# Performance work log

Measured on AMD Instinct MI355X. Metric: run time of the kernel, lower is better.

Reference implementation:

```python
import jax, jax.numpy as jnp
import numpy as np

EMBED_DIM = 1024
NUM_HEADS = 16
HEAD_DIM = EMBED_DIM // NUM_HEADS


def setup_inputs() -> dict:
    key = jax.random.key(0)
    ks = jax.random.split(key, 9)
    B, S, E, Hd = 1, 4096, EMBED_DIM, HEAD_DIM
    s = 0.02
    return {
        "x": jax.random.normal(ks[0], (B, S, E), jnp.float32),
        "mask": jnp.ones((B, S, S), jnp.int32),
        "Wq": jax.random.normal(ks[1], (E, E), jnp.float32) * s,
        "bq": jnp.zeros((E,), jnp.float32),
        "Wk": jax.random.normal(ks[2], (E, Hd), jnp.float32) * s,
        "bk": jnp.zeros((Hd,), jnp.float32),
        "Wv": jax.random.normal(ks[3], (E, Hd), jnp.float32) * s,
        "bv": jnp.zeros((Hd,), jnp.float32),
        "Wo": jax.random.normal(ks[4], (E, E), jnp.float32) * s,
        "bo": jnp.zeros((E,), jnp.float32),
    }


def reference(x, mask, Wq, bq, Wk, bk, Wv, bv, Wo, bo):
    B, S, E = x.shape
    H, Hd = NUM_HEADS, HEAD_DIM
    q = (x @ Wq + bq).reshape(B, S, H, Hd).transpose(0, 2, 1, 3)  # [B,H,S,Hd]
    k = x @ Wk + bk  # [B,S,Hd] single KV head (MQA)
    v = x @ Wv + bv  # [B,S,Hd]
    scale = 1.0 / np.sqrt(Hd).astype(np.float32)
    # broadcast single-head K across all query heads
    qk = jnp.einsum('bhqd,bkd->bhqk', q, k) * scale  # [B,H,S,S]
    qk = jnp.where(mask[:, None, :, :] == 0, jnp.float32(-10000.0), qk)
    attn = jax.nn.softmax(qk, axis=-1)
    out = jnp.einsum('bhqk,bkd->bhqd', attn, v)  # [B,H,S,Hd]
    out = out.transpose(0, 2, 1, 3).reshape(B, S, E)
    return out @ Wo + bo
```

## Files before the change

### kernel.cpp

```cpp
#include <hip/hip_runtime.h>
#include <hip/hip_bf16.h>
#include <stdint.h>

typedef __bf16 bf16x8 __attribute__((ext_vector_type(8)));
typedef float f32x4 __attribute__((ext_vector_type(4)));
typedef float f32x16 __attribute__((ext_vector_type(16)));
typedef unsigned int uint2v __attribute__((ext_vector_type(2)));

#define E_DIM 1024
#define HD 64
#define NH 16
#define QKV_LD 1152
#define LOG2E 1.44269504088896f

__device__ __forceinline__ float toF(float x) { return x; }
__device__ __forceinline__ float toF(__hip_bfloat16 x) { return __bfloat162float(x); }
__device__ __forceinline__ void storeOut(float* p, float v) { *p = v; }
__device__ __forceinline__ void storeOut(__hip_bfloat16* p, float v) { *p = __float2bfloat16(v); }

__device__ __forceinline__ unsigned cvtpk_bf16(float lo, float hi_) {
    unsigned r;
    asm("v_cvt_pk_bf16_f32 %0, %1, %2" : "=v"(r) : "v"(lo), "v"(hi_));
    return r;
}
__device__ __forceinline__ void perm32swap(unsigned& a, unsigned& b) {
    uint2v r = __builtin_amdgcn_permlane32_swap(a, b, false, false);
    a = r.x; b = r.y;
}
__device__ __forceinline__ float fexp2(float x) {
    float r;
    asm("v_exp_f32 %0, %1" : "=v"(r) : "v"(x));
    return r;
}

typedef __attribute__((address_space(1))) void gvoid;
typedef __attribute__((address_space(3))) void lvoid;
__device__ __forceinline__ void gload_lds16(const void* g, void* l) {
    __builtin_amdgcn_global_load_lds((gvoid*)g, (lvoid*)l, 16, 0, 0);
}

__global__ void cast_f32_bf16_kernel(const float* __restrict__ in, __hip_bfloat16* __restrict__ o, int n) {
    int i = (blockIdx.x * blockDim.x + threadIdx.x) * 4;
    if (i + 3 < n) {
        float4 v = *reinterpret_cast<const float4*>(in + i);
        __hip_bfloat16 t[4] = {__float2bfloat16(v.x), __float2bfloat16(v.y),
                               __float2bfloat16(v.z), __float2bfloat16(v.w)};
        *reinterpret_cast<uint2*>(o + i) = *reinterpret_cast<uint2*>(t);
    }
}

template<typename InT>
__global__ void transpose_cast_kernel(const InT* __restrict__ in, int ldi,
                                      __hip_bfloat16* __restrict__ out, int ldo,
                                      int R, int C) {
    __shared__ float tile[32][33];
    const int bx = blockIdx.x * 32;
    const int by = blockIdx.y * 32;
    const int tx = threadIdx.x & 31, ty = threadIdx.x >> 5;
#pragma unroll
    for (int j = 0; j < 4; ++j) {
        int r = bx + ty + j * 8, c = by + tx;
        tile[ty + j * 8][tx] = toF(in[(size_t)r * ldi + c]);
    }
    __syncthreads();
#pragma unroll
    for (int j = 0; j < 4; ++j) {
        int c = by + ty + j * 8, r = bx + tx;
        out[(size_t)c * ldo + r] = __float2bfloat16(tile[tx][ty + j * 8]);
    }
}

__global__ __launch_bounds__(256)
void transpose4_kernel(const float* __restrict__ Wq, const float* __restrict__ Wk,
                       const float* __restrict__ Wv, const float* __restrict__ Wo,
                       __hip_bfloat16* __restrict__ wqkvT, __hip_bfloat16* __restrict__ woT) {
    const int z = blockIdx.z;
    const float* in; __hip_bfloat16* out; int ldi;
    if (z == 0)      { in = Wq; out = wqkvT;                                ldi = E_DIM; }
    else if (z == 1) { if (blockIdx.y >= HD / 32) return;
                       in = Wk; out = wqkvT + (size_t)E_DIM * E_DIM;        ldi = HD; }
    else if (z == 2) { if (blockIdx.y >= HD / 32) return;
                       in = Wv; out = wqkvT + (size_t)(E_DIM + HD) * E_DIM; ldi = HD; }
    else             { in = Wo; out = woT;                                  ldi = E_DIM; }
    __shared__ float tile[32][33];
    const int bx = blockIdx.x * 32;
    const int by = blockIdx.y * 32;
    const int tx = threadIdx.x & 31, ty = threadIdx.x >> 5;
#pragma unroll
    for (int j = 0; j < 4; ++j) {
        int r = bx + ty + j * 8, c = by + tx;
        tile[ty + j * 8][tx] = in[(size_t)r * ldi + c];
    }
    __syncthreads();
#pragma unroll
    for (int j = 0; j < 4; ++j) {
        int c = by + ty + j * 8, r = bx + tx;
        out[(size_t)c * E_DIM + r] = __float2bfloat16(tile[tx][ty + j * 8]);
    }
}

__global__ void concat_bias3_kernel(const float* __restrict__ bq, const float* __restrict__ bk,
                                    const float* __restrict__ bv, float* __restrict__ bqkv) {
    int i = blockIdx.x * blockDim.x + threadIdx.x;
    if (i < E_DIM) bqkv[i] = bq[i];
    else if (i < E_DIM + HD) bqkv[i] = bk[i - E_DIM];
    else if (i < E_DIM + 2 * HD) bqkv[i] = bv[i - E_DIM - HD];
}

__global__ void maskbits_kernel(const int* __restrict__ mask, unsigned long long* __restrict__ mb,
                                int nwords) {
    int gtid = blockIdx.x * blockDim.x + threadIdx.x;
    int wid = gtid >> 6, lane = gtid & 63;
    int nw = (gridDim.x * blockDim.x) >> 6;
    for (int w = wid; w < nwords; w += nw) {
        int v = mask[(size_t)w * 64 + lane];
        unsigned long long b = __ballot(v != 0);
        if (lane == 0) mb[w] = b;
    }
}

template<typename OutT>
__global__ __launch_bounds__(256)
void gemm_bt2_kernel(const __hip_bfloat16* __restrict__ A,
                     const __hip_bfloat16* __restrict__ Bt,
                     const float* __restrict__ bias,
                     OutT* __restrict__ C,
                     int M, int N, int K, float sQ, int nQ, float sKV) {
    constexpr int BM = 128, BN = 128, BK = 64;
    __shared__ __align__(16) unsigned char lA[2][BM * BK * 2];
    __shared__ __align__(16) unsigned char lB[2][BN * BK * 2];
    const int ntn = N / BN;
    const int tm = blockIdx.x / ntn, tn = blockIdx.x % ntn;
    const int tid = threadIdx.x, lane = tid & 63, wave = tid >> 6;
    const int l15 = lane & 15, l4 = lane >> 4;
    const int wm = (wave >> 1) * 64, wn = (wave & 1) * 64;
    const int r0 = tm * BM, c0 = tn * BN;
    const int NK = K / BK;

    size_t aoff[4], boff[4];
    unsigned ldso[4];
#pragma unroll
    for (int i = 0; i < 4; ++i) {
        int row = wave * 32 + i * 8 + (lane >> 3);
        int c = (lane & 7) ^ (row & 7);
        aoff[i] = (size_t)(r0 + row) * K * 2 + c * 16;
        boff[i] = (size_t)(c0 + row) * K * 2 + c * 16;
        ldso[i] = wave * 4096 + i * 1024;
    }
    const char* Ab = (const char*)A;
    const char* Bb = (const char*)Bt;

#pragma unroll
    for (int i = 0; i < 4; ++i) {
        gload_lds16(Ab + aoff[i], &lA[0][ldso[i]]);
        gload_lds16(Bb + boff[i], &lB[0][ldso[i]]);
    }
    __syncthreads();

    f32x4 z4 = {0.f, 0.f, 0.f, 0.f};
    f32x4 acc[4][4];
#pragma unroll
    for (int mi = 0; mi < 4; ++mi)
#pragma unroll
        for (int ni = 0; ni < 4; ++ni) acc[mi][ni] = z4;

    int buf = 0;
    for (int ks = 0; ks < NK; ++ks) {
        if (ks + 1 < NK) {
            size_t kb = (size_t)(ks + 1) * BK * 2;
#pragma unroll
            for (int i = 0; i < 4; ++i) {
                gload_lds16(Ab + aoff[i] + kb, &lA[buf ^ 1][ldso[i]]);
                gload_lds16(Bb + boff[i] + kb, &lB[buf ^ 1][ldso[i]]);
            }
        }
        bf16x8 af[4][2], bf[4][2];
#pragma unroll
        for (int mi = 0; mi < 4; ++mi) {
            int row = wm + mi * 16 + l15;
#pragma unroll
            for (int kh = 0; kh < 2; ++kh) {
                int slot = (kh * 4 + l4) ^ (row & 7);
                af[mi][kh] = *reinterpret_cast<const bf16x8*>(&lA[buf][row * 128 + slot * 16]);
            }
        }
#pragma unroll
        for (int ni = 0; ni < 4; ++ni) {
            int row = wn + ni * 16 + l15;
#pragma unroll
            for (int kh = 0; kh < 2; ++kh) {
                int slot = (kh * 4 + l4) ^ (row & 7);
                bf[ni][kh] = *reinterpret_cast<const bf16x8*>(&lB[buf][row * 128 + slot * 16]);
            }
        }
        __builtin_amdgcn_s_setprio(1);
#pragma unroll
        for (int mi = 0; mi < 4; ++mi)
#pragma unroll
            for (int ni = 0; ni < 4; ++ni) {
                acc[mi][ni] = __builtin_amdgcn_mfma_f32_16x16x32_bf16(af[mi][0], bf[ni][0], acc[mi][ni], 0, 0, 0);
                acc[mi][ni] = __builtin_amdgcn_mfma_f32_16x16x32_bf16(af[mi][1], bf[ni][1], acc[mi][ni], 0, 0, 0);
            }
        __builtin_amdgcn_s_setprio(0);
        __syncthreads();
        buf ^= 1;
    }

#pragma unroll
    for (int ni = 0; ni < 4; ++ni) {
        int col = c0 + wn + ni * 16 + l15;
        float b = bias[col];
        float s = (col < nQ) ? sQ : sKV;
#pragma unroll
        for (int mi = 0; mi < 4; ++mi) {
            int row = r0 + wm + mi * 16 + l4 * 4;
#pragma unroll
            for (int r = 0; r < 4; ++r) {
                float v = (acc[mi][ni][r] + b) * s;
                storeOut(C + (size_t)(row + r) * N + col, v);
            }
        }
    }
}

__global__ __launch_bounds__(256) __attribute__((amdgpu_waves_per_eu(2, 2)))
void mqa7_kernel(const __hip_bfloat16* __restrict__ qkv,
                 const __hip_bfloat16* __restrict__ vtb,
                 const unsigned long long* __restrict__ mbits,
                 __hip_bfloat16* __restrict__ attnb,
                 int S) {
    __shared__ __align__(16) unsigned char sKV[2][32768];
    const int tid = threadIdx.x, lane = tid & 63, w = tid >> 6;
    const int r31 = lane & 31, hi = lane >> 5, rx = r31 & 15;
    const int q0 = blockIdx.x * 32;
    const int h = blockIdx.y * 4 + w;
    const int NT = S / 128, NW64 = S / 64;
    const __hip_bfloat16* kvb = qkv + E_DIM;

    bf16x8 qf[4];
    {
        const __hip_bfloat16* qp = qkv + (size_t)(q0 + r31) * QKV_LD + h * HD + hi * 8;
#pragma unroll
        for (int s = 0; s < 4; ++s) qf[s] = *reinterpret_cast<const bf16x8*>(qp + 16 * s);
    }
    bf16x8 ones;
#pragma unroll
    for (int i = 0; i < 8; ++i) ones[i] = (__bf16)1.0f;

    const char* gbase[8];
    int gstep[8];
    unsigned ldsoff[8];
#pragma unroll
    for (int i = 0; i < 8; ++i) {
        int r = w * 32 + i * 4 + (lane >> 4);
        int sl = lane & 15;
        int c = sl ^ (r & 15);
        if (c < 8) {
            gbase[i] = (const char*)(kvb + (size_t)r * QKV_LD + c * 8);
            gstep[i] = 128 * QKV_LD * 2;
        } else {
            gbase[i] = (const char*)(vtb + (size_t)(r & 63) * S + (r >> 6) * 64 + (c - 8) * 8);
            gstep[i] = 128 * 2;
        }
        ldsoff[i] = w * 8192 + i * 1024;
    }

#pragma unroll
    for (int i = 0; i < 8; ++i) { gload_lds16(gbase[i], &sKV[0][ldsoff[i]]); gbase[i] += gstep[i]; }
    __syncthreads();

    float rm = -3e38f;
    f32x16 oacc[2], lacc;
#pragma unroll
    for (int i = 0; i < 16; ++i) { oacc[0][i] = 0.f; oacc[1][i] = 0.f; lacc[i] = 0.f; }

    const size_t mrow = (size_t)(q0 + r31) * NW64;
    int buf = 0;
    for (int t = 0; t < NT; ++t) {
        ulonglong2 wb = *reinterpret_cast<const ulonglong2*>(mbits + mrow + 2 * t);
        if (t + 1 < NT) {
#pragma unroll
            for (int i = 0; i < 8; ++i) { gload_lds16(gbase[i], &sKV[buf ^ 1][ldsoff[i]]); gbase[i] += gstep[i]; }
        }
        const unsigned char* bp = sKV[buf];

        f32x16 sacc[4];
        __builtin_amdgcn_s_setprio(1);
#pragma unroll
        for (int kb = 0; kb < 4; ++kb) {
            const unsigned char* rowp = bp + (kb * 32 + r31) * 256;
            f32x16 a;
#pragma unroll
            for (int i = 0; i < 16; ++i) a[i] = 0.f;
#pragma unroll
            for (int s = 0; s < 4; ++s) {
                int slot = (2 * s + hi) ^ rx;
                bf16x8 kf = *reinterpret_cast<const bf16x8*>(rowp + slot * 16);
                a = __builtin_amdgcn_mfma_f32_32x32x16_bf16(kf, qf[s], a, 0, 0, 0);
            }
            sacc[kb] = a;
        }
        __builtin_amdgcn_s_setprio(0);

        if ((wb.x & wb.y) != ~0ull) {
#pragma unroll
            for (int kb = 0; kb < 4; ++kb) {
                unsigned long long wv = (kb < 2) ? wb.x : wb.y;
                int base = (kb & 1) * 32;
#pragma unroll
                for (int r = 0; r < 16; ++r) {
                    int kl = base + (r & 3) + 8 * (r >> 2) + 4 * hi;
                    if (!((wv >> kl) & 1)) sacc[kb][r] = -14427.0f;
                }
            }
        }

        float t0[8];
#pragma unroll
        for (int j = 0; j < 8; ++j) {
            float a = fmaxf(fmaxf(sacc[0][j], sacc[0][j + 8]), sacc[1][j]);
            float b = fmaxf(fmaxf(sacc[1][j + 8], sacc[2][j]), sacc[2][j + 8]);
            float c = fmaxf(fmaxf(sacc[3][j], sacc[3][j + 8]), a);
            t0[j] = fmaxf(b, c);
        }
        float u0 = fmaxf(fmaxf(t0[0], t0[1]), t0[2]);
        float u1 = fmaxf(fmaxf(t0[3], t0[4]), t0[5]);
        float pmax = fmaxf(fmaxf(t0[6], t0[7]), fmaxf(u0, u1));

        if (!__all(pmax - rm <= 8.0f)) {
            float pm2 = fmaxf(pmax, __shfl_xor(pmax, 32));
            float rmn = fmaxf(rm, pm2);
            float al = fexp2(rm - rmn);
#pragma unroll
            for (int r = 0; r < 16; ++r) { oacc[0][r] *= al; oacc[1][r] *= al; lacc[r] *= al; }
            rm = rmn;
        }

#pragma unroll
        for (int kb = 0; kb < 4; ++kb)
#pragma unroll
            for (int r = 0; r < 16; ++r) sacc[kb][r] = fexp2(sacc[kb][r] - rm);

#pragma unroll
        for (int j = 0; j < 2; ++j) {
            bf16x8 pa[4];
#pragma unroll
            for (int kk = 0; kk < 2; ++kk) {
#pragma unroll
                for (int half = 0; half < 2; ++half) {
                    int b0 = half * 8;
                    const f32x16& sv = sacc[2 * j + kk];
                    unsigned A = cvtpk_bf16(sv[b0 + 0], sv[b0 + 1]);
                    unsigned B = cvtpk_bf16(sv[b0 + 2], sv[b0 + 3]);
                    unsigned C = cvtpk_bf16(sv[b0 + 4], sv[b0 + 5]);
                    unsigned D = cvtpk_bf16(sv[b0 + 6], sv[b0 + 7]);
                    perm32swap(A, C);
                    perm32swap(B, D);
                    union { unsigned u[4]; bf16x8 v; } pk;
                    pk.u[0] = A; pk.u[1] = B; pk.u[2] = C; pk.u[3] = D;
                    pa[kk * 2 + half] = pk.v;
                }
            }
            __builtin_amdgcn_s_setprio(1);
#pragma unroll
            for (int db = 0; db < 2; ++db) {
                const unsigned char* rowp = bp + (j * 64 + db * 32 + r31) * 256;
                f32x16 a = oacc[db];
#pragma unroll
                for (int s = 0; s < 4; ++s) {
                    int slot = (8 + 2 * s + hi) ^ rx;
                    bf16x8 vf = *reinterpret_cast<const bf16x8*>(rowp + slot * 16);
                    a = __builtin_amdgcn_mfma_f32_32x32x16_bf16(vf, pa[s], a, 0, 0, 0);
                }
                oacc[db] = a;
            }
#pragma unroll
            for (int s = 0; s < 4; ++s)
                lacc = __builtin_amdgcn_mfma_f32_32x32x16_bf16(ones, pa[s], lacc, 0, 0, 0);
            __builtin_amdgcn_s_setprio(0);
        }

        __syncthreads();
        buf ^= 1;
    }

    float inv = 1.0f / lacc[0];
    __hip_bfloat16* op = attnb + (size_t)(q0 + r31) * E_DIM + h * HD;
#pragma unroll
    for (int db = 0; db < 2; ++db)
#pragma unroll
        for (int m = 0; m < 4; ++m) {
            uint2 pk;
            pk.x = cvtpk_bf16(oacc[db][4 * m + 0] * inv, oacc[db][4 * m + 1] * inv);
            pk.y = cvtpk_bf16(oacc[db][4 * m + 2] * inv, oacc[db][4 * m + 3] * inv);
            *reinterpret_cast<uint2*>(op + db * 32 + m * 8 + hi * 4) = pk;
        }
}

extern "C" void kernel_launch(void* const* d_in, const int* in_sizes, int n_in,
                              void* d_out, int out_size, void* d_ws, size_t ws_size,
                              hipStream_t stream) {
    (void)n_in; (void)out_size; (void)ws_size;
    const float* x  = (const float*)d_in[0];
    const int* mask = (const int*)d_in[1];
    const float* Wq = (const float*)d_in[2];
    const float* bq = (const float*)d_in[3];
    const float* Wk = (const float*)d_in[4];
    const float* bk = (const float*)d_in[5];
    const float* Wv = (const float*)d_in[6];
    const float* bv = (const float*)d_in[7];
    const float* Wo = (const float*)d_in[8];
    const float* bo = (const float*)d_in[9];
    float* out = (float*)d_out;

    const int E = E_DIM;
    const int S = in_sizes[0] / E;

    char* ws = (char*)d_ws;
    size_t off = 0;
    auto alloc = [&](size_t b) { char* p = ws + off; off += (b + 255) & ~(size_t)255; return p; };
    __hip_bfloat16* xb     = (__hip_bfloat16*)alloc((size_t)S * E * 2);
    __hip_bfloat16* wqkvT  = (__hip_bfloat16*)alloc((size_t)QKV_LD * E * 2);
    __hip_bfloat16* woT    = (__hip_bfloat16*)alloc((size_t)E * E * 2);
    __hip_bfloat16* qkvb   = (__hip_bfloat16*)alloc((size_t)S * QKV_LD * 2);
    __hip_bfloat16* vtb    = (__hip_bfloat16*)alloc((size_t)HD * S * 2);
    __hip_bfloat16* attnb  = (__hip_bfloat16*)alloc((size_t)S * E * 2);
    float* bqkv  = (float*)alloc(QKV_LD * 4);
    unsigned long long* mbits = (unsigned long long*)alloc((size_t)S * (S / 64) * 8);

    cast_f32_bf16_kernel<<<dim3((S * E / 4 + 255) / 256), dim3(256), 0, stream>>>(x, xb, S * E);
    transpose4_kernel<<<dim3(E / 32, E / 32, 4), dim3(256), 0, stream>>>(Wq, Wk, Wv, Wo, wqkvT, woT);
    concat_bias3_kernel<<<dim3((QKV_LD + 255) / 256), dim3(256), 0, stream>>>(bq, bk, bv, bqkv);
    maskbits_kernel<<<dim3(1024), dim3(256), 0, stream>>>(mask, mbits, S * (S / 64));

    gemm_bt2_kernel<__hip_bfloat16><<<dim3((S / 128) * (QKV_LD / 128)), dim3(256), 0, stream>>>(
        xb, wqkvT, bqkv, qkvb, S, QKV_LD, E, 0.125f * LOG2E, E, 1.0f);
    transpose_cast_kernel<__hip_bfloat16><<<dim3(S / 32, HD / 32), dim3(256), 0, stream>>>(
        qkvb + E + HD, QKV_LD, vtb, S, S, HD);
    mqa7_kernel<<<dim3(S / 32, NH / 4), dim3(256), 0, stream>>>(qkvb, vtb, mbits, attnb, S);
    gemm_bt2_kernel<float><<<dim3((S / 128) * (E / 128)), dim3(256), 0, stream>>>(
        attnb, woT, bo, out, S, E, E, 1.0f, E, 1.0f);
}
```

Before: 176.5 us.

## Split attention tile into two 64-key halves with online softmax per half

The 128-key tile is now processed as two 64-key sub-tiles, each running QK^T, masking, max, rescale, exp and PV before the next starts. This needs two score accumulators live at a time instead of four, lowering register pressure, and the waves_per_eu(2,2) attribute is dropped so the compiler can choose occupancy. A sched_barrier separates the two halves. The cost is twice as many max reductions and rescale checks per tile, and less MFMA work per scheduling window to hide latency.

```diff
diff --git a/kernel.cpp b/kernel.cpp
--- a/kernel.cpp
+++ b/kernel.cpp
@@ -223,8 +223,8 @@
     }
 }
 
-__global__ __launch_bounds__(256) __attribute__((amdgpu_waves_per_eu(2, 2)))
-void mqa7_kernel(const __hip_bfloat16* __restrict__ qkv,
+__global__ __launch_bounds__(256)
+void mqa8_kernel(const __hip_bfloat16* __restrict__ qkv,
                  const __hip_bfloat16* __restrict__ vtb,
                  const unsigned long long* __restrict__ mbits,
                  __hip_bfloat16* __restrict__ attnb,
@@ -284,72 +284,66 @@
         }
         const unsigned char* bp = sKV[buf];
 
-        f32x16 sacc[4];
-        __builtin_amdgcn_s_setprio(1);
-#pragma unroll
-        for (int kb = 0; kb < 4; ++kb) {
-            const unsigned char* rowp = bp + (kb * 32 + r31) * 256;
-            f32x16 a;
-#pragma unroll
-            for (int i = 0; i < 16; ++i) a[i] = 0.f;
-#pragma unroll
-            for (int s = 0; s < 4; ++s) {
-                int slot = (2 * s + hi) ^ rx;
-                bf16x8 kf = *reinterpret_cast<const bf16x8*>(rowp + slot * 16);
-                a = __builtin_amdgcn_mfma_f32_32x32x16_bf16(kf, qf[s], a, 0, 0, 0);
-            }
-            sacc[kb] = a;
-        }
-        __builtin_amdgcn_s_setprio(0);
-
-        if ((wb.x & wb.y) != ~0ull) {
-#pragma unroll
-            for (int kb = 0; kb < 4; ++kb) {
-                unsigned long long wv = (kb < 2) ? wb.x : wb.y;
-                int base = (kb & 1) * 32;
+#pragma unroll
+        for (int j = 0; j < 2; ++j) {
+            unsigned long long wv = j ? wb.y : wb.x;
+
+            f32x16 s0, s1;
+            {
+                const unsigned char* rowp0 = bp + ((2 * j + 0) * 32 + r31) * 256;
+                const unsigned char* rowp1 = bp + ((2 * j + 1) * 32 + r31) * 256;
+                f32x16 a0, a1;
+#pragma unroll
+                for (int i = 0; i < 16; ++i) { a0[i] = 0.f; a1[i] = 0.f; }
+                __builtin_amdgcn_s_setprio(1);
+#pragma unroll
+                for (int s = 0; s < 4; ++s) {
+                    int slot = (2 * s + hi) ^ rx;
+                    bf16x8 k0 = *reinterpret_cast<const bf16x8*>(rowp0 + slot * 16);
+                    bf16x8 k1 = *reinterpret_cast<const bf16x8*>(rowp1 + slot * 16);
+                    a0 = __builtin_amdgcn_mfma_f32_32x32x16_bf16(k0, qf[s], a0, 0, 0, 0);
+                    a1 = __builtin_amdgcn_mfma_f32_32x32x16_bf16(k1, qf[s], a1, 0, 0, 0);
+                }
+                __builtin_amdgcn_s_setprio(0);
+                s0 = a0; s1 = a1;
+            }
+
+            if (wv != ~0ull) {
 #pragma unroll
                 for (int r = 0; r < 16; ++r) {
-                    int kl = base + (r & 3) + 8 * (r >> 2) + 4 * hi;
-                    if (!((wv >> kl) & 1)) sacc[kb][r] = -14427.0f;
+                    int kl = (r & 3) + 8 * (r >> 2) + 4 * hi;
+                    if (!((wv >> kl) & 1)) s0[r] = -14427.0f;
+                    if (!((wv >> (kl + 32)) & 1)) s1[r] = -14427.0f;
                 }
             }
-        }
-
-        float t0[8];
-#pragma unroll
-        for (int j = 0; j < 8; ++j) {
-            float a = fmaxf(fmaxf(sacc[0][j], sacc[0][j + 8]), sacc[1][j]);
-            float b = fmaxf(fmaxf(sacc[1][j + 8], sacc[2][j]), sacc[2][j + 8]);
-            float c = fmaxf(fmaxf(sacc[3][j], sacc[3][j + 8]), a);
-            t0[j] = fmaxf(b, c);
-        }
-        float u0 = fmaxf(fmaxf(t0[0], t0[1]), t0[2]);
-        float u1 = fmaxf(fmaxf(t0[3], t0[4]), t0[5]);
-        float pmax = fmaxf(fmaxf(t0[6], t0[7]), fmaxf(u0, u1));
-
-        if (!__all(pmax - rm <= 8.0f)) {
-            float pm2 = fmaxf(pmax, __shfl_xor(pmax, 32));
-            float rmn = fmaxf(rm, pm2);
-            float al = fexp2(rm - rmn);
-#pragma unroll
-            for (int r = 0; r < 16; ++r) { oacc[0][r] *= al; oacc[1][r] *= al; lacc[r] *= al; }
-            rm = rmn;
-        }
-
-#pragma unroll
-        for (int kb = 0; kb < 4; ++kb)
-#pragma unroll
-            for (int r = 0; r < 16; ++r) sacc[kb][r] = fexp2(sacc[kb][r] - rm);
-
-#pragma unroll
-        for (int j = 0; j < 2; ++j) {
+
+            float t0[8];
+#pragma unroll
+            for (int js = 0; js < 8; ++js)
+                t0[js] = fmaxf(fmaxf(s0[js], s0[js + 8]), fmaxf(s1[js], s1[js + 8]));
+            float u0 = fmaxf(fmaxf(t0[0], t0[4]), fmaxf(t0[1], t0[5]));
+            float u1 = fmaxf(fmaxf(t0[2], t0[6]), fmaxf(t0[3], t0[7]));
+            float pmax = fmaxf(u0, u1);
+
+            if (!__all(pmax - rm <= 8.0f)) {
+                float pm2 = fmaxf(pmax, __shfl_xor(pmax, 32));
+                float rmn = fmaxf(rm, pm2);
+                float al = fexp2(rm - rmn);
+#pragma unroll
+                for (int r = 0; r < 16; ++r) { oacc[0][r] *= al; oacc[1][r] *= al; lacc[r] *= al; }
+                rm = rmn;
+            }
+
+#pragma unroll
+            for (int r = 0; r < 16; ++r) { s0[r] = fexp2(s0[r] - rm); s1[r] = fexp2(s1[r] - rm); }
+
             bf16x8 pa[4];
 #pragma unroll
             for (int kk = 0; kk < 2; ++kk) {
+                const f32x16& sv = kk ? s1 : s0;
 #pragma unroll
                 for (int half = 0; half < 2; ++half) {
                     int b0 = half * 8;
-                    const f32x16& sv = sacc[2 * j + kk];
                     unsigned A = cvtpk_bf16(sv[b0 + 0], sv[b0 + 1]);
                     unsigned B = cvtpk_bf16(sv[b0 + 2], sv[b0 + 3]);
                     unsigned C = cvtpk_bf16(sv[b0 + 4], sv[b0 + 5]);
@@ -361,6 +355,7 @@
                     pa[kk * 2 + half] = pk.v;
                 }
             }
+
             __builtin_amdgcn_s_setprio(1);
 #pragma unroll
             for (int db = 0; db < 2; ++db) {
@@ -378,6 +373,8 @@
             for (int s = 0; s < 4; ++s)
                 lacc = __builtin_amdgcn_mfma_f32_32x32x16_bf16(ones, pa[s], lacc, 0, 0, 0);
             __builtin_amdgcn_s_setprio(0);
+
+            __builtin_amdgcn_sched_barrier(0);
         }
 
         __syncthreads();
@@ -437,7 +434,7 @@
         xb, wqkvT, bqkv, qkvb, S, QKV_LD, E, 0.125f * LOG2E, E, 1.0f);
     transpose_cast_kernel<__hip_bfloat16><<<dim3(S / 32, HD / 32), dim3(256), 0, stream>>>(
         qkvb + E + HD, QKV_LD, vtb, S, S, HD);
-    mqa7_kernel<<<dim3(S / 32, NH / 4), dim3(256), 0, stream>>>(qkvb, vtb, mbits, attnb, S);
+    mqa8_kernel<<<dim3(S / 32, NH / 4), dim3(256), 0, stream>>>(qkvb, vtb, mbits, attnb, S);
     gemm_bt2_kernel<float><<<dim3((S / 128) * (E / 128)), dim3(256), 0, stream>>>(
         attnb, woT, bo, out, S, E, E, 1.0f, E, 1.0f);
 }
```

Result: slower. 232.5 us (+31.7%).
